# Kernel optimization log

Measured on AMD Instinct MI355X. Metric: run time of the kernel, lower is better.

The kernel has to match this reference:

```python
import jax, jax.numpy as jnp
import numpy as np

N, E = 10000, 320000
F_N, F_E, F_G, LATENT, F_OUT = 128, 128, 32, 128, 128


def _make_mlp_params(key, dims):
    # dims: list of layer widths, e.g. [256,128,128,128,256]
    params = []
    for i in range(len(dims) - 1):
        key, k1, k2 = jax.random.split(key, 3)
        lim = 1.0 / np.sqrt(dims[i])
        w = jax.random.uniform(k1, (dims[i], dims[i + 1]), jnp.float32, -lim, lim)
        b = jax.random.uniform(k2, (dims[i + 1],), jnp.float32, -lim, lim)
        params.append((w, b))
    return params, key


def _mlp(h, ws, bs, activate_final):
    n = len(ws)
    for i in range(n):
        h = h @ ws[i] + bs[i]
        if i < n - 1 or activate_final:
            h = jax.nn.relu(h)
    return h


def setup_inputs() -> dict:
    key = jax.random.key(0)
    key, kx, ke, kg, ki = jax.random.split(key, 5)
    x = jax.random.normal(kx, (N, F_N), jnp.float32)
    edge_index = jax.random.randint(ki, (2, E), 0, N, jnp.int64)
    edge_attr = jax.random.normal(ke, (E, F_E), jnp.float32)
    global_attr = jax.random.normal(kg, (1, F_G), jnp.float32)

    # node_mlp_1: (F_N+F_E) -> L -> L -> L -> (F_N+F_E), activate_final=True
    p1, key = _make_mlp_params(key, [F_N + F_E, LATENT, LATENT, LATENT, F_N + F_E])
    # node_mlp_2: (2*F_N+F_E+F_G) -> L -> L -> L -> F_OUT, activate_final=False
    p2, key = _make_mlp_params(key, [2 * F_N + F_E + F_G, LATENT, LATENT, LATENT, F_OUT])

    inp = {"x": x, "edge_index": edge_index, "edge_attr": edge_attr, "global_attr": global_attr}
    for i, (w, b) in enumerate(p1):
        inp[f"m1_w{i}"] = w
        inp[f"m1_b{i}"] = b
    for i, (w, b) in enumerate(p2):
        inp[f"m2_w{i}"] = w
        inp[f"m2_b{i}"] = b
    return inp


def reference(x, edge_index, edge_attr, global_attr,
              m1_w0, m1_b0, m1_w1, m1_b1, m1_w2, m1_b2, m1_w3, m1_b3,
              m2_w0, m2_b0, m2_w1, m2_b1, m2_w2, m2_b2, m2_w3, m2_b3):
    row, col = edge_index[0], edge_index[1]
    n = x.shape[0]
    # gather sender-side node feats, per-edge MLP (activate_final=True)
    h = jnp.concatenate([x[row], edge_attr], axis=1)          # [E, F_N+F_E]
    h = _mlp(h, [m1_w0, m1_w1, m1_w2, m1_w3], [m1_b0, m1_b1, m1_b2, m1_b3], True)
    # scatter_mean over destination nodes
    s = jax.ops.segment_sum(h, col, num_segments=n)           # [N, F_N+F_E]
    cnt = jax.ops.segment_sum(jnp.ones((h.shape[0],), h.dtype), col, num_segments=n)
    agg = s / jnp.maximum(cnt, 1.0)[:, None]
    # repeat global feats to N rows (pad_to_size mode='repeat', G divides N)
    g = jnp.tile(global_attr, (n // global_attr.shape[0], 1))  # [N, F_G]
    out = jnp.concatenate([x, agg, g], axis=1)                 # [N, 2F_N+F_E+F_G]
    return _mlp(out, [m2_w0, m2_w1, m2_w2, m2_w3], [m2_b0, m2_b1, m2_b2, m2_b3], False)
```

## Files before the change

kernel.cpp:

```cpp
#include <hip/hip_runtime.h>
#include <hip/hip_bf16.h>

#define E_EDGES 320000
#define N_NODES 10000

typedef __attribute__((ext_vector_type(8))) short short8;
typedef __attribute__((ext_vector_type(4))) float floatx4;

__device__ __forceinline__ float bf2f(unsigned short u) {
    union { unsigned int i; float f; } v; v.i = ((unsigned int)u) << 16; return v.f;
}
__device__ __forceinline__ unsigned int pk2(float a, float b) {
    float2 t; t.x = a; t.y = b;
    __hip_bfloat162 h = __float22bfloat162_rn(t);
    union { __hip_bfloat162 h; unsigned int u; } c; c.h = h; return c.u;
}

template<int K, int Nn, int FT, int ET>
__device__ __forceinline__ void layer_acc(const unsigned short* __restrict__ in, int istride,
                                          const unsigned short* __restrict__ wt,
                                          int lane, int n0, floatx4 (&acc)[FT][ET])
{
    const int quad = lane >> 4;
    const int mrow = lane & 15;
    floatx4 zero = {0.f, 0.f, 0.f, 0.f};
#pragma unroll
    for (int ft = 0; ft < FT; ++ft)
#pragma unroll
        for (int et = 0; et < ET; ++et)
            acc[ft][et] = zero;

#pragma unroll
    for (int kt = 0; kt < K / 32; ++kt) {
        const int koff = kt * 32 + quad * 8;
        short8 a[FT];
        short8 b[ET];
#pragma unroll
        for (int ft = 0; ft < FT; ++ft)
            a[ft] = *(const short8*)&wt[(size_t)(kt * (Nn >> 4) + (n0 >> 4) + ft) * 512 + lane * 8];
#pragma unroll
        for (int et = 0; et < ET; ++et)
            b[et] = *(const short8*)&in[(et * 16 + mrow) * istride + koff];
#pragma unroll
        for (int ft = 0; ft < FT; ++ft)
#pragma unroll
            for (int et = 0; et < ET; ++et)
                acc[ft][et] = __builtin_amdgcn_mfma_f32_16x16x32_bf16(a[ft], b[et], acc[ft][et], 0, 0, 0);
    }
}

template<int FT, int ET>
__device__ __forceinline__ void store_lds(floatx4 (&acc)[FT][ET], const float* __restrict__ bias,
                                          int lane, int n0, unsigned short* __restrict__ out, int ostride,
                                          bool relu)
{
    const int quad = lane >> 4, mrow = lane & 15;
#pragma unroll
    for (int ft = 0; ft < FT; ++ft) {
        int fbase = n0 + ft * 16 + quad * 4;
        float4 bv = *(const float4*)&bias[fbase];
#pragma unroll
        for (int et = 0; et < ET; ++et) {
            int edge = et * 16 + mrow;
            float v0 = acc[ft][et][0] + bv.x;
            float v1 = acc[ft][et][1] + bv.y;
            float v2 = acc[ft][et][2] + bv.z;
            float v3 = acc[ft][et][3] + bv.w;
            if (relu) {
                v0 = v0 > 0.f ? v0 : 0.f; v1 = v1 > 0.f ? v1 : 0.f;
                v2 = v2 > 0.f ? v2 : 0.f; v3 = v3 > 0.f ? v3 : 0.f;
            }
            uint2 pk; pk.x = pk2(v0, v1); pk.y = pk2(v2, v3);
            *(uint2*)&out[edge * ostride + fbase] = pk;
        }
    }
}

struct TDesc { const float* src; unsigned short* dst; int nElem; int logN; int blockStart; };
struct TArgs { TDesc d[8]; };

__global__ void prep_kernel(TArgs a, const int* __restrict__ eidx, int* __restrict__ cnt, int histStart)
{
    int b = blockIdx.x;
    if (b >= histStart) {
        int e = (b - histStart) * 256 + threadIdx.x;
        if (e < E_EDGES) atomicAdd(&cnt[eidx[E_EDGES + e]], 1);
        return;
    }
    int i = 0;
#pragma unroll
    for (int j = 1; j < 8; ++j)
        if (b >= a.d[j].blockStart) i = j;
    const TDesc t = a.d[i];
    int idx = (b - t.blockStart) * 256 + threadIdx.x;
    if (idx < t.nElem) {
        int n = idx & ((1 << t.logN) - 1);
        int k = idx >> t.logN;
        int ntiles = 1 << (t.logN - 4);
        size_t dsti = ((size_t)(k >> 5) * ntiles + (n >> 4)) * 512
                    + ((k >> 3) & 3) * 128 + (n & 15) * 8 + (k & 7);
        union { float f; unsigned int u; } c; c.f = t.src[idx];
        unsigned int uu = c.u;
        t.dst[dsti] = (unsigned short)((uu + 0x7fffu + ((uu >> 16) & 1u)) >> 16);
    }
}

__global__ void scan_kernel(const int* __restrict__ cnt, int* __restrict__ fill)
{
    __shared__ int partial[256];
    const int CH = 40;
    int tid = threadIdx.x;
    int base = tid * CH;
    int local[CH];
    int sum = 0;
#pragma unroll
    for (int j = 0; j < CH; ++j) {
        int idx = base + j;
        int c = (idx < N_NODES) ? cnt[idx] : 0;
        local[j] = c;
        sum += c;
    }
    partial[tid] = sum;
    __syncthreads();
    for (int o = 1; o < 256; o <<= 1) {
        int v = (tid >= o) ? partial[tid - o] : 0;
        __syncthreads();
        partial[tid] += v;
        __syncthreads();
    }
    int run = partial[tid] - sum;
#pragma unroll
    for (int j = 0; j < CH; ++j) {
        int idx = base + j;
        if (idx < N_NODES) fill[idx] = run;
        run += local[j];
    }
}

__global__ void fill_kernel(const int* __restrict__ eidx, int* __restrict__ fill,
                            int* __restrict__ elist, int* __restrict__ rowp, int* __restrict__ dstp)
{
    int e = blockIdx.x * 256 + threadIdx.x;
    int c = eidx[E_EDGES + e];
    int r = eidx[e];
    int pos = atomicAdd(&fill[c], 1);
    elist[pos] = e;
    rowp[pos] = r;
    dstp[pos] = c;
}

__global__ __launch_bounds__(256, 3) void edge_kernel(
    const float* __restrict__ x,
    const float* __restrict__ ea,
    const int* __restrict__ elist, const int* __restrict__ rowp, const int* __restrict__ dstp,
    const unsigned short* __restrict__ wt0, const float* __restrict__ b0,
    const unsigned short* __restrict__ wt1, const float* __restrict__ b1,
    const unsigned short* __restrict__ wt2, const float* __restrict__ b2,
    const unsigned short* __restrict__ wt3, const float* __restrict__ b3,
    float* __restrict__ s)
{
    __shared__ __align__(16) char U[51200];
    __shared__ int es[64];
    __shared__ int rs[64];
    __shared__ int ds[64];

    unsigned short* H0 = (unsigned short*)U;
    unsigned short* H1 = (unsigned short*)(U + 33792);
    unsigned short* H2 = (unsigned short*)U;
    unsigned short* H3 = H1;
    unsigned short* G  = (unsigned short*)U;

    const int tid = threadIdx.x;
    const int p0 = blockIdx.x * 64;

    if (tid < 64) {
        es[tid] = elist[p0 + tid];
        rs[tid] = rowp[p0 + tid];
        ds[tid] = dstp[p0 + tid];
    }
    __syncthreads();

#pragma unroll
    for (int i = 0; i < 16; ++i) {
        int task = tid + i * 256;
        int row = task >> 6, part = task & 63;
        float4 v;
        if (part < 32) v = *(const float4*)(x + (size_t)rs[row] * 128 + part * 4);
        else           v = *(const float4*)(ea + (size_t)es[row] * 128 + (part - 32) * 4);
        uint2 pk; pk.x = pk2(v.x, v.y); pk.y = pk2(v.z, v.w);
        *(uint2*)&H0[row * 264 + part * 4] = pk;
    }
    __syncthreads();

    const int lane = tid & 63;
    const int wave = tid >> 6;

    {
        floatx4 acc[2][4];
        layer_acc<256, 128, 2, 4>(H0, 264, wt0, lane, wave * 32, acc);
        store_lds<2, 4>(acc, b0, lane, wave * 32, H1, 136, true);
    }
    __syncthreads();
    {
        floatx4 acc[2][4];
        layer_acc<128, 128, 2, 4>(H1, 136, wt1, lane, wave * 32, acc);
        store_lds<2, 4>(acc, b1, lane, wave * 32, H2, 136, true);
    }
    __syncthreads();
    {
        floatx4 acc[2][4];
        layer_acc<128, 128, 2, 4>(H2, 136, wt2, lane, wave * 32, acc);
        store_lds<2, 4>(acc, b2, lane, wave * 32, H3, 136, true);
    }
    __syncthreads();
    {
        floatx4 acc[4][4];
        layer_acc<128, 256, 4, 4>(H3, 136, wt3, lane, wave * 64, acc);
        store_lds<4, 4>(acc, b3, lane, wave * 64, G, 264, true);
    }
    __syncthreads();

    {
        int p = tid & 127;
        int half = tid >> 7;
        int col2 = p * 2;
        int base = half * 32;
        float s0 = 0.f, s1 = 0.f;
#pragma unroll 4
        for (int i = 0; i < 32; ++i) {
            int gi = base + i;
            unsigned int u = *(const unsigned int*)&G[gi * 264 + col2];
            s0 += bf2f((unsigned short)u);
            s1 += bf2f((unsigned short)(u >> 16));
            if (i == 31 || ds[gi + 1] != ds[gi]) {
                float* dst = &s[(size_t)ds[gi] * 256 + col2];
                atomicAdd(dst, s0);
                atomicAdd(dst + 1, s1);
                s0 = 0.f; s1 = 0.f;
            }
        }
    }
}

__global__ __launch_bounds__(256, 2) void node_kernel(
    const float* __restrict__ x,
    const float* __restrict__ g,
    const float* __restrict__ s,
    const int* __restrict__ cnt,
    const unsigned short* __restrict__ wt0, const float* __restrict__ b0,
    const unsigned short* __restrict__ wt1, const float* __restrict__ b1,
    const unsigned short* __restrict__ wt2, const float* __restrict__ b2,
    const unsigned short* __restrict__ wt3, const float* __restrict__ b3,
    float* __restrict__ out)
{
    __shared__ __align__(16) char NU[71680];
    unsigned short* Abig = (unsigned short*)NU;
    unsigned short* HsA  = (unsigned short*)(NU + 54272);
    unsigned short* HsB  = (unsigned short*)NU;

    const int tid = threadIdx.x;
    const int node0 = blockIdx.x * 64;

#pragma unroll
    for (int i = 0; i < 8; ++i) {
        int task = tid + i * 256;
        int row = task >> 5, part = task & 31;
        int node = node0 + row;
        uint2 pk = {0u, 0u};
        if (node < N_NODES) {
            float4 v = *(const float4*)(x + (size_t)node * 128 + part * 4);
            pk.x = pk2(v.x, v.y); pk.y = pk2(v.z, v.w);
        }
        *(uint2*)&Abig[row * 424 + part * 4] = pk;
    }
#pragma unroll
    for (int i = 0; i < 16; ++i) {
        int task = tid + i * 256;
        int row = task >> 6, part = task & 63;
        int node = node0 + row;
        uint2 pk = {0u, 0u};
        if (node < N_NODES) {
            float c = (float)cnt[node];
            float inv = 1.f / (c > 1.f ? c : 1.f);
            floatx4 v = *(const floatx4*)(s + (size_t)node * 256 + part * 4);
            pk.x = pk2(v[0] * inv, v[1] * inv);
            pk.y = pk2(v[2] * inv, v[3] * inv);
        }
        *(uint2*)&Abig[row * 424 + 128 + part * 4] = pk;
    }
#pragma unroll
    for (int i = 0; i < 2; ++i) {
        int task = tid + i * 256;
        int row = task >> 3, part = task & 7;
        float4 v = *(const float4*)(g + part * 4);
        uint2 pk; pk.x = pk2(v.x, v.y); pk.y = pk2(v.z, v.w);
        *(uint2*)&Abig[row * 424 + 384 + part * 4] = pk;
    }
    __syncthreads();

    const int lane = tid & 63;
    const int wave = tid >> 6;

    {
        floatx4 acc[2][4];
        layer_acc<416, 128, 2, 4>(Abig, 424, wt0, lane, wave * 32, acc);
        store_lds<2, 4>(acc, b0, lane, wave * 32, HsA, 136, true);
    }
    __syncthreads();
    {
        floatx4 acc[2][4];
        layer_acc<128, 128, 2, 4>(HsA, 136, wt1, lane, wave * 32, acc);
        store_lds<2, 4>(acc, b1, lane, wave * 32, HsB, 136, true);
    }
    __syncthreads();
    {
        floatx4 acc[2][4];
        layer_acc<128, 128, 2, 4>(HsB, 136, wt2, lane, wave * 32, acc);
        store_lds<2, 4>(acc, b2, lane, wave * 32, HsA, 136, true);
    }
    __syncthreads();
    {
        floatx4 acc[2][4];
        layer_acc<128, 128, 2, 4>(HsA, 136, wt3, lane, wave * 32, acc);
        const int quad = lane >> 4, mrow = lane & 15;
#pragma unroll
        for (int ft = 0; ft < 2; ++ft) {
            int fbase = wave * 32 + ft * 16 + quad * 4;
            float4 bv = *(const float4*)&b3[fbase];
#pragma unroll
            for (int et = 0; et < 4; ++et) {
                int node = node0 + et * 16 + mrow;
                if (node < N_NODES) {
                    float4 o;
                    o.x = acc[ft][et][0] + bv.x;
                    o.y = acc[ft][et][1] + bv.y;
                    o.z = acc[ft][et][2] + bv.z;
                    o.w = acc[ft][et][3] + bv.w;
                    *(float4*)&out[(size_t)node * 128 + fbase] = o;
                }
            }
        }
    }
}

extern "C" void kernel_launch(void* const* d_in, const int* in_sizes, int n_in,
                              void* d_out, int out_size, void* d_ws, size_t ws_size,
                              hipStream_t stream)
{
    (void)in_sizes; (void)n_in; (void)out_size; (void)ws_size;

    const float* x  = (const float*)d_in[0];
    const int* eidx = (const int*)d_in[1];
    const float* ea = (const float*)d_in[2];
    const float* g  = (const float*)d_in[3];

    const float* w1[4]  = { (const float*)d_in[4],  (const float*)d_in[6],
                            (const float*)d_in[8],  (const float*)d_in[10] };
    const float* bb1[4] = { (const float*)d_in[5],  (const float*)d_in[7],
                            (const float*)d_in[9],  (const float*)d_in[11] };
    const float* w2[4]  = { (const float*)d_in[12], (const float*)d_in[14],
                            (const float*)d_in[16], (const float*)d_in[18] };
    const float* bb2[4] = { (const float*)d_in[13], (const float*)d_in[15],
                            (const float*)d_in[17], (const float*)d_in[19] };

    char* p = (char*)d_ws;
    unsigned short* wt1_0 = (unsigned short*)p; p += 256 * 128 * 2;
    unsigned short* wt1_1 = (unsigned short*)p; p += 128 * 128 * 2;
    unsigned short* wt1_2 = (unsigned short*)p; p += 128 * 128 * 2;
    unsigned short* wt1_3 = (unsigned short*)p; p += 128 * 256 * 2;
    unsigned short* wt2_0 = (unsigned short*)p; p += 416 * 128 * 2;
    unsigned short* wt2_1 = (unsigned short*)p; p += 128 * 128 * 2;
    unsigned short* wt2_2 = (unsigned short*)p; p += 128 * 128 * 2;
    unsigned short* wt2_3 = (unsigned short*)p; p += 128 * 128 * 2;
    float* s   = (float*)p; p += (size_t)N_NODES * 256 * 4;
    int* cnt   = (int*)p;   p += (size_t)N_NODES * 4;
    int* fill  = (int*)p;   p += (size_t)N_NODES * 4;
    int* elist = (int*)p;   p += (size_t)E_EDGES * 4;
    int* rowp  = (int*)p;   p += (size_t)E_EDGES * 4;
    int* dstp  = (int*)p;   p += (size_t)E_EDGES * 4;

    hipMemsetAsync(s, 0, (size_t)N_NODES * 256 * 4 + (size_t)N_NODES * 4, stream);

    TArgs ta;
    int bs = 0;
    auto set = [&](int i, const float* src, unsigned short* dst, int K, int Nn, int logN) {
        ta.d[i].src = src; ta.d[i].dst = dst; ta.d[i].nElem = K * Nn;
        ta.d[i].logN = logN; ta.d[i].blockStart = bs;
        bs += (K * Nn + 255) / 256;
    };
    set(0, w1[0], wt1_0, 256, 128, 7);
    set(1, w1[1], wt1_1, 128, 128, 7);
    set(2, w1[2], wt1_2, 128, 128, 7);
    set(3, w1[3], wt1_3, 128, 256, 8);
    set(4, w2[0], wt2_0, 416, 128, 7);
    set(5, w2[1], wt2_1, 128, 128, 7);
    set(6, w2[2], wt2_2, 128, 128, 7);
    set(7, w2[3], wt2_3, 128, 128, 7);

    int histBlocks = E_EDGES / 256;
    hipLaunchKernelGGL(prep_kernel, dim3(bs + histBlocks), dim3(256), 0, stream,
                       ta, eidx, cnt, bs);
    hipLaunchKernelGGL(scan_kernel, dim3(1), dim3(256), 0, stream, cnt, fill);
    hipLaunchKernelGGL(fill_kernel, dim3(E_EDGES / 256), dim3(256), 0, stream,
                       eidx, fill, elist, rowp, dstp);

    hipLaunchKernelGGL(edge_kernel, dim3(E_EDGES / 64), dim3(256), 0, stream,
                       x, ea, elist, rowp, dstp,
                       wt1_0, bb1[0], wt1_1, bb1[1], wt1_2, bb1[2], wt1_3, bb1[3],
                       s);

    hipLaunchKernelGGL(node_kernel, dim3((N_NODES + 63) / 64), dim3(256), 0, stream,
                       x, g, s, cnt,
                       wt2_0, bb2[0], wt2_1, bb2[1], wt2_2, bb2[2], wt2_3, bb2[3],
                       (float*)d_out);
}
```

Baseline: 479.0 us.

## Prefetch MFMA weight fragments, double-buffer LDS operands, and halve node-kernel tile

Rewrites the per-layer MFMA loop so weight fragments for all K tiles are loaded into registers up front, and the LDS activation fragments are double-buffered so the next K tile's loads overlap the current MFMAs. A streaming variant that double-buffers both operands is used for the wide first node layer. The last edge layer is split into two 32-column passes to cap register pressure. The node kernel now handles 32 nodes per block with half the LDS and a higher occupancy bound, giving more blocks and better latency hiding at the cost of re-reading weights more often.

```diff
diff --git a/kernel.cpp b/kernel.cpp
--- a/kernel.cpp
+++ b/kernel.cpp
@@ -16,36 +16,107 @@
     union { __hip_bfloat162 h; unsigned int u; } c; c.h = h; return c.u;
 }
 
-template<int K, int Nn, int FT, int ET>
-__device__ __forceinline__ void layer_acc(const unsigned short* __restrict__ in, int istride,
+template<int K, int Nn, int ET, bool BDB>
+__device__ __forceinline__ void layer_pre(const unsigned short* __restrict__ in, int istride,
                                           const unsigned short* __restrict__ wt,
-                                          int lane, int n0, floatx4 (&acc)[FT][ET])
-{
+                                          int lane, int n0, floatx4 (&acc)[2][ET])
+{
+    constexpr int KT = K / 32;
     const int quad = lane >> 4;
     const int mrow = lane & 15;
+
+    short8 a[KT][2];
+#pragma unroll
+    for (int kt = 0; kt < KT; ++kt)
+#pragma unroll
+        for (int ft = 0; ft < 2; ++ft)
+            a[kt][ft] = *(const short8*)&wt[(size_t)(kt * (Nn >> 4) + (n0 >> 4) + ft) * 512 + lane * 8];
+
     floatx4 zero = {0.f, 0.f, 0.f, 0.f};
 #pragma unroll
-    for (int ft = 0; ft < FT; ++ft)
+    for (int ft = 0; ft < 2; ++ft)
 #pragma unroll
         for (int et = 0; et < ET; ++et)
             acc[ft][et] = zero;
 
-#pragma unroll
-    for (int kt = 0; kt < K / 32; ++kt) {
-        const int koff = kt * 32 + quad * 8;
-        short8 a[FT];
-        short8 b[ET];
-#pragma unroll
-        for (int ft = 0; ft < FT; ++ft)
-            a[ft] = *(const short8*)&wt[(size_t)(kt * (Nn >> 4) + (n0 >> 4) + ft) * 512 + lane * 8];
+    if constexpr (BDB) {
+        short8 b[2][ET];
 #pragma unroll
         for (int et = 0; et < ET; ++et)
-            b[et] = *(const short8*)&in[(et * 16 + mrow) * istride + koff];
-#pragma unroll
-        for (int ft = 0; ft < FT; ++ft)
+            b[0][et] = *(const short8*)&in[(et * 16 + mrow) * istride + quad * 8];
+#pragma unroll
+        for (int kt = 0; kt < KT; ++kt) {
+            if (kt + 1 < KT) {
+                const int koff = (kt + 1) * 32 + quad * 8;
+#pragma unroll
+                for (int et = 0; et < ET; ++et)
+                    b[(kt + 1) & 1][et] = *(const short8*)&in[(et * 16 + mrow) * istride + koff];
+            }
+#pragma unroll
+            for (int ft = 0; ft < 2; ++ft)
+#pragma unroll
+                for (int et = 0; et < ET; ++et)
+                    acc[ft][et] = __builtin_amdgcn_mfma_f32_16x16x32_bf16(a[kt][ft], b[kt & 1][et], acc[ft][et], 0, 0, 0);
+        }
+    } else {
+#pragma unroll
+        for (int kt = 0; kt < KT; ++kt) {
+            const int koff = kt * 32 + quad * 8;
+            short8 b[ET];
 #pragma unroll
             for (int et = 0; et < ET; ++et)
-                acc[ft][et] = __builtin_amdgcn_mfma_f32_16x16x32_bf16(a[ft], b[et], acc[ft][et], 0, 0, 0);
+                b[et] = *(const short8*)&in[(et * 16 + mrow) * istride + koff];
+#pragma unroll
+            for (int ft = 0; ft < 2; ++ft)
+#pragma unroll
+                for (int et = 0; et < ET; ++et)
+                    acc[ft][et] = __builtin_amdgcn_mfma_f32_16x16x32_bf16(a[kt][ft], b[et], acc[ft][et], 0, 0, 0);
+        }
+    }
+}
+
+template<int K, int Nn, int ET>
+__device__ __forceinline__ void layer_stream(const unsigned short* __restrict__ in, int istride,
+                                             const unsigned short* __restrict__ wt,
+                                             int lane, int n0, floatx4 (&acc)[2][ET])
+{
+    constexpr int KT = K / 32;
+    const int quad = lane >> 4;
+    const int mrow = lane & 15;
+
+    floatx4 zero = {0.f, 0.f, 0.f, 0.f};
+#pragma unroll
+    for (int ft = 0; ft < 2; ++ft)
+#pragma unroll
+        for (int et = 0; et < ET; ++et)
+            acc[ft][et] = zero;
+
+    short8 a[2][2];
+    short8 b[2][ET];
+#pragma unroll
+    for (int ft = 0; ft < 2; ++ft)
+        a[0][ft] = *(const short8*)&wt[(size_t)((n0 >> 4) + ft) * 512 + lane * 8];
+#pragma unroll
+    for (int et = 0; et < ET; ++et)
+        b[0][et] = *(const short8*)&in[(et * 16 + mrow) * istride + quad * 8];
+
+#pragma unroll
+    for (int kt = 0; kt < KT; ++kt) {
+        if (kt + 1 < KT) {
+            const int nb = (kt + 1) & 1;
+            const int koff = (kt + 1) * 32 + quad * 8;
+#pragma unroll
+            for (int ft = 0; ft < 2; ++ft)
+                a[nb][ft] = *(const short8*)&wt[(size_t)((kt + 1) * (Nn >> 4) + (n0 >> 4) + ft) * 512 + lane * 8];
+#pragma unroll
+            for (int et = 0; et < ET; ++et)
+                b[nb][et] = *(const short8*)&in[(et * 16 + mrow) * istride + koff];
+        }
+#pragma unroll
+        for (int ft = 0; ft < 2; ++ft)
+#pragma unroll
+            for (int et = 0; et < ET; ++et)
+                acc[ft][et] = __builtin_amdgcn_mfma_f32_16x16x32_bf16(a[kt & 1][ft], b[kt & 1][et], acc[ft][et], 0, 0, 0);
     }
 }
 
@@ -197,26 +268,29 @@
 
     {
         floatx4 acc[2][4];
-        layer_acc<256, 128, 2, 4>(H0, 264, wt0, lane, wave * 32, acc);
+        layer_pre<256, 128, 4, false>(H0, 264, wt0, lane, wave * 32, acc);
         store_lds<2, 4>(acc, b0, lane, wave * 32, H1, 136, true);
     }
     __syncthreads();
     {
         floatx4 acc[2][4];
-        layer_acc<128, 128, 2, 4>(H1, 136, wt1, lane, wave * 32, acc);
+        layer_pre<128, 128, 4, true>(H1, 136, wt1, lane, wave * 32, acc);
         store_lds<2, 4>(acc, b1, lane, wave * 32, H2, 136, true);
     }
     __syncthreads();
     {
         floatx4 acc[2][4];
-        layer_acc<128, 128, 2, 4>(H2, 136, wt2, lane, wave * 32, acc);
+        layer_pre<128, 128, 4, true>(H2, 136, wt2, lane, wave * 32, acc);
         store_lds<2, 4>(acc, b2, lane, wave * 32, H3, 136, true);
     }
     __syncthreads();
     {
-        floatx4 acc[4][4];
-        layer_acc<128, 256, 4, 4>(H3, 136, wt3, lane, wave * 64, acc);
-        store_lds<4, 4>(acc, b3, lane, wave * 64, G, 264, true);
+        floatx4 acc[2][4];
+        layer_pre<128, 256, 4, true>(H3, 136, wt3, lane, wave * 64, acc);
+        store_lds<2, 4>(acc, b3, lane, wave * 64, G, 264, true);
+        floatx4 acc2[2][4];
+        layer_pre<128, 256, 4, true>(H3, 136, wt3, lane, wave * 64 + 32, acc2);
+        store_lds<2, 4>(acc2, b3, lane, wave * 64 + 32, G, 264, true);
     }
     __syncthreads();
 
@@ -242,7 +316,7 @@
     }
 }
 
-__global__ __launch_bounds__(256, 2) void node_kernel(
+__global__ __launch_bounds__(256, 4) void node_kernel(
     const float* __restrict__ x,
     const float* __restrict__ g,
     const float* __restrict__ s,
@@ -253,16 +327,16 @@
     const unsigned short* __restrict__ wt3, const float* __restrict__ b3,
     float* __restrict__ out)
 {
-    __shared__ __align__(16) char NU[71680];
+    __shared__ __align__(16) char NU[35840];
     unsigned short* Abig = (unsigned short*)NU;
-    unsigned short* HsA  = (unsigned short*)(NU + 54272);
+    unsigned short* HsA  = (unsigned short*)(NU + 27136);
     unsigned short* HsB  = (unsigned short*)NU;
 
     const int tid = threadIdx.x;
-    const int node0 = blockIdx.x * 64;
-
-#pragma unroll
-    for (int i = 0; i < 8; ++i) {
+    const int node0 = blockIdx.x * 32;
+
+#pragma unroll
+    for (int i = 0; i < 4; ++i) {
         int task = tid + i * 256;
         int row = task >> 5, part = task & 31;
         int node = node0 + row;
@@ -274,7 +348,7 @@
         *(uint2*)&Abig[row * 424 + part * 4] = pk;
     }
 #pragma unroll
-    for (int i = 0; i < 16; ++i) {
+    for (int i = 0; i < 8; ++i) {
         int task = tid + i * 256;
         int row = task >> 6, part = task & 63;
         int node = node0 + row;
@@ -288,9 +362,8 @@
         }
         *(uint2*)&Abig[row * 424 + 128 + part * 4] = pk;
     }
-#pragma unroll
-    for (int i = 0; i < 2; ++i) {
-        int task = tid + i * 256;
+    {
+        int task = tid;
         int row = task >> 3, part = task & 7;
         float4 v = *(const float4*)(g + part * 4);
         uint2 pk; pk.x = pk2(v.x, v.y); pk.y = pk2(v.z, v.w);
@@ -302,33 +375,33 @@
     const int wave = tid >> 6;
 
     {
-        floatx4 acc[2][4];
-        layer_acc<416, 128, 2, 4>(Abig, 424, wt0, lane, wave * 32, acc);
-        store_lds<2, 4>(acc, b0, lane, wave * 32, HsA, 136, true);
-    }
-    __syncthreads();
-    {
-        floatx4 acc[2][4];
-        layer_acc<128, 128, 2, 4>(HsA, 136, wt1, lane, wave * 32, acc);
-        store_lds<2, 4>(acc, b1, lane, wave * 32, HsB, 136, true);
-    }
-    __syncthreads();
-    {
-        floatx4 acc[2][4];
-        layer_acc<128, 128, 2, 4>(HsB, 136, wt2, lane, wave * 32, acc);
-        store_lds<2, 4>(acc, b2, lane, wave * 32, HsA, 136, true);
-    }
-    __syncthreads();
-    {
-        floatx4 acc[2][4];
-        layer_acc<128, 128, 2, 4>(HsA, 136, wt3, lane, wave * 32, acc);
+        floatx4 acc[2][2];
+        layer_stream<416, 128, 2>(Abig, 424, wt0, lane, wave * 32, acc);
+        store_lds<2, 2>(acc, b0, lane, wave * 32, HsA, 136, true);
+    }
+    __syncthreads();
+    {
+        floatx4 acc[2][2];
+        layer_pre<128, 128, 2, true>(HsA, 136, wt1, lane, wave * 32, acc);
+        store_lds<2, 2>(acc, b1, lane, wave * 32, HsB, 136, true);
+    }
+    __syncthreads();
+    {
+        floatx4 acc[2][2];
+        layer_pre<128, 128, 2, true>(HsB, 136, wt2, lane, wave * 32, acc);
+        store_lds<2, 2>(acc, b2, lane, wave * 32, HsA, 136, true);
+    }
+    __syncthreads();
+    {
+        floatx4 acc[2][2];
+        layer_pre<128, 128, 2, true>(HsA, 136, wt3, lane, wave * 32, acc);
         const int quad = lane >> 4, mrow = lane & 15;
 #pragma unroll
         for (int ft = 0; ft < 2; ++ft) {
             int fbase = wave * 32 + ft * 16 + quad * 4;
             float4 bv = *(const float4*)&b3[fbase];
 #pragma unroll
-            for (int et = 0; et < 4; ++et) {
+            for (int et = 0; et < 2; ++et) {
                 int node = node0 + et * 16 + mrow;
                 if (node < N_NODES) {
                     float4 o;
@@ -409,7 +482,7 @@
                        wt1_0, bb1[0], wt1_1, bb1[1], wt1_2, bb1[2], wt1_3, bb1[3],
                        s);
 
-    hipLaunchKernelGGL(node_kernel, dim3((N_NODES + 63) / 64), dim3(256), 0, stream,
+    hipLaunchKernelGGL(node_kernel, dim3((N_NODES + 31) / 32), dim3(256), 0, stream,
                        x, g, s, cnt,
                        wt2_0, bb2[0], wt2_1, bb2[1], wt2_2, bb2[2], wt2_3, bb2[3],
                        (float*)d_out);
```

Result: no change. 477.1 us (-0.4%).
